# Kernel tuning notes

Hardware: AMD Instinct MI355X
Metric: run time of the kernel (lower is better)

Reference implementation:

```python
import jax, jax.numpy as jnp
import numpy as np

N, E, F, H, L, G = 100000, 1600000, 128, 128, 8, 256
EPS = 1e-5


def setup_inputs() -> dict:
    key = jax.random.key(0)
    ks = jax.random.split(key, 12)
    s = 0.05
    return {
        "x": jax.random.normal(ks[0], (N, F), jnp.float32),
        "edge_index": jax.random.randint(ks[1], (2, E), 0, N, dtype=jnp.int32),
        "batch": jnp.sort(jax.random.randint(ks[2], (N,), 0, G, dtype=jnp.int32)),
        # input projection
        "Wp": jax.random.normal(ks[3], (F, H), jnp.float32) * s,
        "bp": jnp.zeros((H,), jnp.float32),
        # stacked residual-block params (L blocks, 2 GCNConv+BN each)
        "W1": jax.random.normal(ks[4], (L, H, H), jnp.float32) * s,
        "b1": jnp.zeros((L, H), jnp.float32),
        "g1": jnp.ones((L, H), jnp.float32),
        "be1": jnp.zeros((L, H), jnp.float32),
        "W2": jax.random.normal(ks[5], (L, H, H), jnp.float32) * s,
        "b2": jnp.zeros((L, H), jnp.float32),
        "g2": jnp.ones((L, H), jnp.float32),
        "be2": jnp.zeros((L, H), jnp.float32),
        # readout MLP: 3H -> 2H -> H -> 1
        "Wa": jax.random.normal(ks[6], (3 * H, 2 * H), jnp.float32) * s,
        "ba": jnp.zeros((2 * H,), jnp.float32),
        "Wb": jax.random.normal(ks[7], (2 * H, H), jnp.float32) * s,
        "bb": jnp.zeros((H,), jnp.float32),
        "Wc": jax.random.normal(ks[8], (H, 1), jnp.float32) * s,
        "bc": jnp.zeros((1,), jnp.float32),
    }


def _bn(h, g, b):
    # BatchNorm over the node dimension (training-style batch stats, eps=1e-5)
    mu = h.mean(0)
    var = h.var(0)
    return (h - mu) * jax.lax.rsqrt(var + EPS) * g + b


def reference(x, edge_index, batch, Wp, bp, W1, b1, g1, be1, W2, b2, g2, be2,
              Wa, ba, Wb, bb, Wc, bc):
    src, dst = edge_index[0], edge_index[1]
    # GCN symmetric norm with self-loops: deg = in-degree + 1
    deg = jnp.zeros((N,), x.dtype).at[dst].add(1.0) + 1.0
    dinv = jax.lax.rsqrt(deg)
    norm_e = (dinv[src] * dinv[dst])[:, None]   # [E,1]
    self_norm = (dinv * dinv)[:, None]          # [N,1]

    def gcn(h, W, b):
        hw = h @ W                                              # [N,H]
        agg = jnp.zeros_like(hw).at[dst].add(norm_e * hw[src])  # scatter-add over edges
        return agg + self_norm * hw + b                         # self-loop + bias

    h = x @ Wp + bp

    def step(h, p):
        w1, bb1, gg1, bbe1, w2, bb2, gg2, bbe2 = p
        o = jax.nn.relu(_bn(gcn(h, w1, bb1), gg1, bbe1))
        o = _bn(gcn(o, w2, bb2), gg2, bbe2)
        return h + o, None

    h, _ = jax.lax.scan(step, h, (W1, b1, g1, be1, W2, b2, g2, be2))

    sums = jax.ops.segment_sum(h, batch, num_segments=G)
    cnt = jax.ops.segment_sum(jnp.ones((N, 1), h.dtype), batch, num_segments=G)
    mean = sums / jnp.maximum(cnt, 1.0)
    mx = jax.ops.segment_max(h, batch, num_segments=G)
    z = jnp.concatenate([mean, mx, sums], axis=1)  # [G, 3H]

    z = jax.nn.relu(z @ Wa + ba)
    z = jax.nn.relu(z @ Wb + bb)
    return z @ Wc + bc  # [G, 1]
```

## Files before the change

kernel.cpp:

```cpp
#include <hip/hip_runtime.h>
#include <hip/hip_fp16.h>
#include <math.h>
#include <float.h>

#define HDIM 128
#define NGRAPH 256
#define EPSBN 1e-5f
#define PS_REP 32
#define SLABF (2 * PS_REP * 128)

typedef _Float16 f16x8 __attribute__((ext_vector_type(8)));
typedef _Float16 f16x4 __attribute__((ext_vector_type(4)));
typedef float f32x4 __attribute__((ext_vector_type(4)));

__device__ inline unsigned enc_f(float v) {
  unsigned u = __float_as_uint(v);
  return (u & 0x80000000u) ? ~u : (u | 0x80000000u);
}
__device__ inline float dec_f(unsigned e) {
  return __uint_as_float((e & 0x80000000u) ? (e ^ 0x80000000u) : ~e);
}

__global__ void k_deg(const int* __restrict__ dst, int* __restrict__ deg, int E) {
  int i = blockIdx.x * blockDim.x + threadIdx.x;
  if (i < E) atomicAdd(&deg[dst[i]], 1);
}

__global__ void k_dinv(const int* __restrict__ deg, float* __restrict__ dinv, int n) {
  int i = blockIdx.x * blockDim.x + threadIdx.x;
  if (i < n) dinv[i] = rsqrtf((float)deg[i] + 1.0f);
}

__global__ void k_scanA(const int* __restrict__ deg, int* __restrict__ rowstart,
                        int* __restrict__ bsum, int n) {
  __shared__ int s[256];
  int t = threadIdx.x, i = blockIdx.x * 256 + t;
  int v = (i < n) ? ((deg[i] + 7) & ~7) : 0;
  s[t] = v;
  __syncthreads();
  for (int off = 1; off < 256; off <<= 1) {
    int x = (t >= off) ? s[t - off] : 0;
    __syncthreads();
    s[t] += x;
    __syncthreads();
  }
  if (i < n) rowstart[i] = s[t] - v;
  if (t == 255) bsum[blockIdx.x] = s[255];
}

__global__ void k_scanB(int* __restrict__ bsum, int nb) {
  __shared__ int s[512];
  int t = threadIdx.x;
  int v = (t < nb) ? bsum[t] : 0;
  s[t] = v;
  __syncthreads();
  for (int off = 1; off < 512; off <<= 1) {
    int x = (t >= off) ? s[t - off] : 0;
    __syncthreads();
    s[t] += x;
    __syncthreads();
  }
  if (t < nb) bsum[t] = s[t] - v;
}

__global__ void k_scanC(int* __restrict__ rowstart, const int* __restrict__ bsum,
                        const int* __restrict__ deg, int n) {
  int i = blockIdx.x * 256 + threadIdx.x;
  if (i < n) {
    int v = rowstart[i] + bsum[blockIdx.x];
    rowstart[i] = v;
    if (i == n - 1) rowstart[n] = v + ((deg[i] + 7) & ~7);
  }
}

__global__ void k_fill(const int* __restrict__ src, const int* __restrict__ dst,
                       const float* __restrict__ dinv, const int* __restrict__ prow,
                       int* __restrict__ cursor, int2* __restrict__ csr_sw, int E) {
  int e = blockIdx.x * blockDim.x + threadIdx.x;
  if (e < E) {
    int d = dst[e], s = src[e];
    int pos = prow[d] + atomicAdd(&cursor[d], 1);
    csr_sw[pos] = make_int2(s, __float_as_int(dinv[s] * dinv[d]));
  }
}

__global__ void k_pad(const int* __restrict__ deg, const int* __restrict__ prow,
                      int2* __restrict__ csr_sw, int n) {
  int i = blockIdx.x * blockDim.x + threadIdx.x;
  if (i < n) {
    int d = deg[i], dp = (d + 7) & ~7;
    int base = prow[i];
    for (int j = d; j < dp; ++j) csr_sw[base + j] = make_int2(i, 0);
  }
}

__global__ __launch_bounds__(256) void k_wprep(const float* __restrict__ W1,
                                               const float* __restrict__ W2,
                                               const float* __restrict__ Wp,
                                               _Float16* __restrict__ wt) {
  int m = blockIdx.x;
  const float* Wsrc = (m == 16) ? Wp : (((m & 1) ? W2 : W1) + (size_t)(m >> 1) * 16384);
  _Float16* Wdst = wt + (size_t)m * 16384;
  __shared__ _Float16 lds[128 * 132];
  int t = threadIdx.x;
  const float4* W4 = (const float4*)Wsrc;
  for (int it = 0; it < 16; ++it) {
    int idx = t + it * 256;
    int k = idx >> 5, c4 = idx & 31;
    float4 v = W4[idx];
    lds[(c4 * 4 + 0) * 132 + k] = (_Float16)v.x;
    lds[(c4 * 4 + 1) * 132 + k] = (_Float16)v.y;
    lds[(c4 * 4 + 2) * 132 + k] = (_Float16)v.z;
    lds[(c4 * 4 + 3) * 132 + k] = (_Float16)v.w;
  }
  __syncthreads();
  for (int it = 0; it < 16; ++it) {
    int idx = t + it * 256;
    int col = idx >> 5, k4 = idx & 31;
    f16x4 o;
    o[0] = lds[col * 132 + k4 * 4 + 0];
    o[1] = lds[col * 132 + k4 * 4 + 1];
    o[2] = lds[col * 132 + k4 * 4 + 2];
    o[3] = lds[col * 132 + k4 * 4 + 3];
    *(f16x4*)(Wdst + col * 128 + k4 * 4) = o;
  }
}

__global__ __launch_bounds__(256) void k_gemmp(const float* __restrict__ in,
                                               const _Float16* __restrict__ wt,
                                               const float* __restrict__ bias,
                                               float* __restrict__ out, int n) {
  __shared__ _Float16 As[64 * 128];
  __shared__ _Float16 Bs[128 * 128];
  char* Ap = (char*)As;
  char* Bp = (char*)Bs;
  int tid = threadIdx.x;
  int lane = tid & 63;
  int rt = tid >> 6;
  int row0 = blockIdx.x * 64;

  for (int it = 0; it < 8; ++it) {
    int idx = tid + it * 256;
    int r = idx >> 5, c4 = idx & 31;
    int row = row0 + r;
    if (row >= n) row = n - 1;
    float4 v = *(const float4*)(in + (size_t)row * 128 + c4 * 4);
    f16x4 hv;
    hv[0] = (_Float16)v.x; hv[1] = (_Float16)v.y;
    hv[2] = (_Float16)v.z; hv[3] = (_Float16)v.w;
    *(f16x4*)(Ap + ((r * 256 + c4 * 8) ^ ((r & 7) << 4))) = hv;
  }
  for (int it = 0; it < 8; ++it) {
    int idx = tid + it * 256;
    int col = idx >> 4, k8 = idx & 15;
    f16x8 v = *(const f16x8*)(wt + col * 128 + k8 * 8);
    *(f16x8*)(Bp + ((col * 256 + k8 * 16) ^ ((col & 7) << 4))) = v;
  }
  __syncthreads();

  f32x4 acc[8];
#pragma unroll
  for (int ct = 0; ct < 8; ++ct) acc[ct] = (f32x4){0.f, 0.f, 0.f, 0.f};
  int arow = rt * 16 + (lane & 15);
  int kc = (lane >> 4) * 16;
#pragma unroll
  for (int ks = 0; ks < 4; ++ks) {
    int kb = ks * 64;
    f16x8 a = *(f16x8*)(Ap + ((arow * 256 + kb + kc) ^ ((arow & 7) << 4)));
#pragma unroll
    for (int ct = 0; ct < 8; ++ct) {
      int bcol = ct * 16 + (lane & 15);
      f16x8 b = *(f16x8*)(Bp + ((bcol * 256 + kb + kc) ^ ((bcol & 7) << 4)));
      acc[ct] = __builtin_amdgcn_mfma_f32_16x16x32_f16(a, b, acc[ct], 0, 0, 0);
    }
  }

  int orow0 = row0 + rt * 16 + (lane >> 4) * 4;
#pragma unroll
  for (int ct = 0; ct < 8; ++ct) {
    int col = ct * 16 + (lane & 15);
    float bb = bias[col];
#pragma unroll
    for (int r = 0; r < 4; ++r) {
      int row = orow0 + r;
      if (row < n) out[(size_t)row * 128 + col] = acc[ct][r] + bb;
    }
  }
}

template <int XFORM>
__global__ __launch_bounds__(256) void k_gemmh(const float* __restrict__ in,
                                               const _Float16* __restrict__ wt,
                                               const float* __restrict__ psumL,
                                               const float* __restrict__ gg,
                                               const float* __restrict__ be,
                                               float* __restrict__ hres,
                                               _Float16* __restrict__ outh, int n) {
  __shared__ _Float16 As[64 * 128];
  __shared__ _Float16 Bs[128 * 128];
  __shared__ float sc_s[128], sh_s[128];
  char* Ap = (char*)As;
  char* Bp = (char*)Bs;
  int tid = threadIdx.x;
  int lane = tid & 63;
  int rt = tid >> 6;
  int row0 = blockIdx.x * 64;

  if (XFORM) {
    if (tid < 128) {
      const float* psqL = psumL + PS_REP * 128;
      float s = 0.f, q = 0.f;
#pragma unroll 8
      for (int r = 0; r < PS_REP; ++r) {
        s += psumL[r * 128 + tid];
        q += psqL[r * 128 + tid];
      }
      float mu = s / (float)n;
      float var = q / (float)n - mu * mu;
      float rs = rsqrtf(var + EPSBN);
      float sc = gg[tid] * rs;
      sc_s[tid] = sc;
      sh_s[tid] = be[tid] - mu * sc;
    }
    __syncthreads();
  }

  for (int it = 0; it < 8; ++it) {
    int idx = tid + it * 256;
    int r = idx >> 5, c4 = idx & 31;
    int rrow = row0 + r;
    int row = (rrow >= n) ? (n - 1) : rrow;
    float4 v = *(const float4*)(in + (size_t)row * 128 + c4 * 4);
    if (XFORM == 1) {
      float4 sc = *(const float4*)(sc_s + c4 * 4);
      float4 sh = *(const float4*)(sh_s + c4 * 4);
      v.x = fmaxf(v.x * sc.x + sh.x, 0.f);
      v.y = fmaxf(v.y * sc.y + sh.y, 0.f);
      v.z = fmaxf(v.z * sc.z + sh.z, 0.f);
      v.w = fmaxf(v.w * sc.w + sh.w, 0.f);
    }
    if (XFORM == 2) {
      float4 sc = *(const float4*)(sc_s + c4 * 4);
      float4 sh = *(const float4*)(sh_s + c4 * 4);
      float4 hv = *(const float4*)(hres + (size_t)row * 128 + c4 * 4);
      v.x = v.x * sc.x + sh.x + hv.x;
      v.y = v.y * sc.y + sh.y + hv.y;
      v.z = v.z * sc.z + sh.z + hv.z;
      v.w = v.w * sc.w + sh.w + hv.w;
      if (rrow < n) *(float4*)(hres + (size_t)row * 128 + c4 * 4) = v;
    }
    f16x4 hv16;
    hv16[0] = (_Float16)v.x; hv16[1] = (_Float16)v.y;
    hv16[2] = (_Float16)v.z; hv16[3] = (_Float16)v.w;
    *(f16x4*)(Ap + ((r * 256 + c4 * 8) ^ ((r & 7) << 4))) = hv16;
  }
  for (int it = 0; it < 8; ++it) {
    int idx = tid + it * 256;
    int col = idx >> 4, k8 = idx & 15;
    f16x8 v = *(const f16x8*)(wt + col * 128 + k8 * 8);
    *(f16x8*)(Bp + ((col * 256 + k8 * 16) ^ ((col & 7) << 4))) = v;
  }
  __syncthreads();

  f32x4 acc[8];
#pragma unroll
  for (int ct = 0; ct < 8; ++ct) acc[ct] = (f32x4){0.f, 0.f, 0.f, 0.f};

  int arow = rt * 16 + (lane & 15);
  int kc = (lane >> 4) * 16;
#pragma unroll
  for (int ks = 0; ks < 4; ++ks) {
    int kb = ks * 64;
    f16x8 a = *(f16x8*)(Ap + ((arow * 256 + kb + kc) ^ ((arow & 7) << 4)));
#pragma unroll
    for (int ct = 0; ct < 8; ++ct) {
      int bcol = ct * 16 + (lane & 15);
      f16x8 b = *(f16x8*)(Bp + ((bcol * 256 + kb + kc) ^ ((bcol & 7) << 4)));
      acc[ct] = __builtin_amdgcn_mfma_f32_16x16x32_f16(a, b, acc[ct], 0, 0, 0);
    }
  }

  int orow0 = row0 + rt * 16 + (lane >> 4) * 4;
#pragma unroll
  for (int ct = 0; ct < 8; ++ct) {
    int col = ct * 16 + (lane & 15);
#pragma unroll
    for (int r = 0; r < 4; ++r) {
      int row = orow0 + r;
      if (row < n) outh[(size_t)row * 128 + col] = (_Float16)acc[ct][r];
    }
  }
}

__global__ __launch_bounds__(256) void k_agg(const _Float16* __restrict__ hw,
                                             const int* __restrict__ prow,
                                             const int4* __restrict__ csr4,
                                             const float* __restrict__ dinv,
                                             const float* __restrict__ bias,
                                             float* __restrict__ out,
                                             float* __restrict__ psumL, int n) {
  int wave = threadIdx.x >> 6;
  int lane = threadIdx.x & 63;
  int grp = lane >> 4;
  int l16 = lane & 15;
  int node = blockIdx.x * 4 + wave;
  float a[8];
#pragma unroll
  for (int j = 0; j < 8; ++j) a[j] = 0.f;

  if (node < n) {
    float b8[8];
#pragma unroll
    for (int j = 0; j < 8; ++j) b8[j] = 0.f;
    int q0 = prow[node] >> 1, q1 = prow[node + 1] >> 1;
    for (int q = q0; q < q1; q += 4) {
      int4 p0 = csr4[q], p1 = csr4[q + 1], p2 = csr4[q + 2], p3 = csr4[q + 3];
      int4 pa = (grp & 2) ? p1 : p0;
      int4 pb = (grp & 2) ? p3 : p2;
      int sa = (grp & 1) ? pa.z : pa.x;
      float wa = __int_as_float((grp & 1) ? pa.w : pa.y);
      int sb = (grp & 1) ? pb.z : pb.x;
      float wb = __int_as_float((grp & 1) ? pb.w : pb.y);
      f16x8 va = *(const f16x8*)(hw + (size_t)sa * 128 + l16 * 8);
      f16x8 vb = *(const f16x8*)(hw + (size_t)sb * 128 + l16 * 8);
#pragma unroll
      for (int j = 0; j < 8; ++j) {
        a[j] += wa * (float)va[j];
        b8[j] += wb * (float)vb[j];
      }
    }
#pragma unroll
    for (int j = 0; j < 8; ++j) a[j] += b8[j];
#pragma unroll
    for (int j = 0; j < 8; ++j) {
      a[j] += __shfl_xor(a[j], 16);
      a[j] += __shfl_xor(a[j], 32);
    }
    float dn = dinv[node];
    float sn = dn * dn;
    f16x8 v = *(const f16x8*)(hw + (size_t)node * 128 + l16 * 8);
    float4 bb0 = *(const float4*)(bias + l16 * 8);
    float4 bb1 = *(const float4*)(bias + l16 * 8 + 4);
    a[0] += sn * (float)v[0] + bb0.x;
    a[1] += sn * (float)v[1] + bb0.y;
    a[2] += sn * (float)v[2] + bb0.z;
    a[3] += sn * (float)v[3] + bb0.w;
    a[4] += sn * (float)v[4] + bb1.x;
    a[5] += sn * (float)v[5] + bb1.y;
    a[6] += sn * (float)v[6] + bb1.z;
    a[7] += sn * (float)v[7] + bb1.w;
    if (grp == 0) {
      *(float4*)(out + (size_t)node * 128 + l16 * 8) = make_float4(a[0], a[1], a[2], a[3]);
      *(float4*)(out + (size_t)node * 128 + l16 * 8 + 4) = make_float4(a[4], a[5], a[6], a[7]);
    }
  }
  __shared__ float ss[4][128];
  __shared__ float sq[4][128];
  if (grp == 0) {
    bool live = (node < n);
#pragma unroll
    for (int j = 0; j < 8; ++j) {
      float v = live ? a[j] : 0.f;
      ss[wave][l16 * 8 + j] = v;
      sq[wave][l16 * 8 + j] = v * v;
    }
  }
  __syncthreads();
  int t = threadIdx.x;
  if (t < 128) {
    float s = (ss[0][t] + ss[1][t]) + (ss[2][t] + ss[3][t]);
    float q = (sq[0][t] + sq[1][t]) + (sq[2][t] + sq[3][t]);
    int rep = blockIdx.x & (PS_REP - 1);
    atomicAdd(&psumL[rep * 128 + t], s);
    atomicAdd(&psumL[PS_REP * 128 + rep * 128 + t], q);
  }
}

#define PCHUNK 128
__global__ __launch_bounds__(128) void k_pool(const float* __restrict__ h,
                                              const float* __restrict__ t2,
                                              const float* __restrict__ psumL,
                                              const float* __restrict__ gg,
                                              const float* __restrict__ be,
                                              const int* __restrict__ batch,
                                              float* __restrict__ sums,
                                              unsigned* __restrict__ maxenc,
                                              int* __restrict__ cnt, int n) {
  int c = threadIdx.x;
  __shared__ float sc_s[128], sh_s[128];
  {
    const float* psqL = psumL + PS_REP * 128;
    float s = 0.f, q = 0.f;
#pragma unroll 8
    for (int r = 0; r < PS_REP; ++r) {
      s += psumL[r * 128 + c];
      q += psqL[r * 128 + c];
    }
    float mu = s / (float)n;
    float var = q / (float)n - mu * mu;
    float rs = rsqrtf(var + EPSBN);
    float sc = gg[c] * rs;
    sc_s[c] = sc;
    sh_s[c] = be[c] - mu * sc;
  }
  __syncthreads();
  float scc = sc_s[c], shc = sh_s[c];

  int start = blockIdx.x * PCHUNK;
  if (start >= n) return;
  int end = start + PCHUNK;
  if (end > n) end = n;
  int cur = batch[start];
  float s = 0.f, mx = -FLT_MAX;
  int runlen = 0;
  for (int i = start; i < end; ++i) {
    int b = batch[i];
    if (b != cur) {
      atomicAdd(&sums[cur * 128 + c], s);
      atomicMax(&maxenc[cur * 128 + c], enc_f(mx));
      if (c == 0) atomicAdd(&cnt[cur], runlen);
      s = 0.f; mx = -FLT_MAX; runlen = 0; cur = b;
    }
    float v = h[(size_t)i * 128 + c] + scc * t2[(size_t)i * 128 + c] + shc;
    s += v;
    mx = fmaxf(mx, v);
    runlen++;
  }
  atomicAdd(&sums[cur * 128 + c], s);
  atomicMax(&maxenc[cur * 128 + c], enc_f(mx));
  if (c == 0) atomicAdd(&cnt[cur], runlen);
}

__global__ __launch_bounds__(256) void k_readout(const float* __restrict__ sums,
                                                 const unsigned* __restrict__ maxenc,
                                                 const int* __restrict__ cnt,
                                                 const float* __restrict__ Wa,
                                                 const float* __restrict__ ba,
                                                 const float* __restrict__ Wb,
                                                 const float* __restrict__ bb,
                                                 const float* __restrict__ Wc,
                                                 const float* __restrict__ bc,
                                                 float* __restrict__ out) {
  int g = blockIdx.x;
  int t = threadIdx.x;
  __shared__ float z[384];
  __shared__ float za[256];
  __shared__ float zb[128];
  float c = (float)(cnt[g] > 1 ? cnt[g] : 1);
  if (t < 128) {
    float s = sums[g * 128 + t];
    z[t] = s / c;
    z[128 + t] = dec_f(maxenc[g * 128 + t]);
    z[256 + t] = s;
  }
  __syncthreads();
  float accA = ba[t];
  for (int k = 0; k < 384; k++) accA += z[k] * Wa[k * 256 + t];
  za[t] = fmaxf(accA, 0.f);
  __syncthreads();
  if (t < 128) {
    float accB = bb[t];
    for (int k = 0; k < 256; k++) accB += za[k] * Wb[k * 128 + t];
    zb[t] = fmaxf(accB, 0.f);
  }
  __syncthreads();
  if (t < 64) {
    float p = zb[t] * Wc[t] + zb[t + 64] * Wc[t + 64];
    for (int off = 32; off > 0; off >>= 1) p += __shfl_down(p, off);
    if (t == 0) out[g] = p + bc[0];
  }
}

extern "C" void kernel_launch(void* const* d_in, const int* in_sizes, int n_in,
                              void* d_out, int out_size, void* d_ws, size_t ws_size,
                              hipStream_t stream) {
  const float* x   = (const float*)d_in[0];
  const int* edge  = (const int*)d_in[1];
  const int* batch = (const int*)d_in[2];
  const float* Wp  = (const float*)d_in[3];
  const float* bp  = (const float*)d_in[4];
  const float* W1  = (const float*)d_in[5];
  const float* b1  = (const float*)d_in[6];
  const float* g1  = (const float*)d_in[7];
  const float* be1 = (const float*)d_in[8];
  const float* W2  = (const float*)d_in[9];
  const float* b2  = (const float*)d_in[10];
  const float* g2  = (const float*)d_in[11];
  const float* be2 = (const float*)d_in[12];
  const float* Wa  = (const float*)d_in[13];
  const float* ba  = (const float*)d_in[14];
  const float* Wb  = (const float*)d_in[15];
  const float* bbp = (const float*)d_in[16];
  const float* Wc  = (const float*)d_in[17];
  const float* bc  = (const float*)d_in[18];
  float* out = (float*)d_out;

  const int N = in_sizes[0] / 128;
  const int E = in_sizes[1] / 2;
  const int* esrc = edge;
  const int* edst = edge + E;

  char* p = (char*)d_ws;
  auto carve = [&](size_t bytes) {
    char* r = p;
    p += (bytes + 255) & ~(size_t)255;
    return (void*)r;
  };
  float* h    = (float*)carve((size_t)N * 128 * 4);
  _Float16* t1h = (_Float16*)carve((size_t)N * 128 * 2);
  float* t2   = (float*)carve((size_t)N * 128 * 4);
  int2* csr_sw = (int2*)carve(((size_t)E + 8 * (size_t)N) * 8);
  int* deg     = (int*)carve((size_t)N * 4);
  float* dinv  = (float*)carve((size_t)N * 4);
  int* prow    = (int*)carve((size_t)(N + 1) * 4);
  int* cursor  = (int*)carve((size_t)N * 4);
  int* bsum    = (int*)carve(512 * 4);
  float* slab  = (float*)carve((size_t)16 * SLABF * 4);
  float* pools = (float*)carve((size_t)NGRAPH * 128 * 4);
  unsigned* poolm = (unsigned*)carve((size_t)NGRAPH * 128 * 4);
  int* poolc      = (int*)carve(NGRAPH * 4);
  _Float16* wt16  = (_Float16*)carve((size_t)17 * 128 * 128 * 2);

  const int NB = (N + 255) / 256;

  hipMemsetAsync(deg, 0, (size_t)N * 4, stream);
  hipMemsetAsync(cursor, 0, (size_t)N * 4, stream);
  hipMemsetAsync(slab, 0, (size_t)16 * SLABF * 4, stream);
  hipMemsetAsync(pools, 0, (size_t)NGRAPH * 128 * 4, stream);
  hipMemsetAsync(poolm, 0, (size_t)NGRAPH * 128 * 4, stream);
  hipMemsetAsync(poolc, 0, (size_t)NGRAPH * 4, stream);

  k_deg<<<(E + 255) / 256, 256, 0, stream>>>(edst, deg, E);
  k_dinv<<<NB, 256, 0, stream>>>(deg, dinv, N);
  k_scanA<<<NB, 256, 0, stream>>>(deg, prow, bsum, N);
  k_scanB<<<1, 512, 0, stream>>>(bsum, NB);
  k_scanC<<<NB, 256, 0, stream>>>(prow, bsum, deg, N);
  k_fill<<<(E + 255) / 256, 256, 0, stream>>>(esrc, edst, dinv, prow, cursor, csr_sw, E);
  k_pad<<<NB, 256, 0, stream>>>(deg, prow, csr_sw, N);
  k_wprep<<<17, 256, 0, stream>>>(W1, W2, Wp, wt16);

  const int GB = (N + 63) / 64;
  const int AB = (N + 3) / 4;
  const int PB = (N + PCHUNK - 1) / PCHUNK;

  k_gemmp<<<GB, 256, 0, stream>>>(x, wt16 + (size_t)16 * 16384, bp, h, N);
  k_gemmh<0><<<GB, 256, 0, stream>>>(h, wt16, nullptr, nullptr, nullptr, nullptr, t1h, N);

  for (int l = 0; l < 8; l++) {
    const _Float16* w2t = wt16 + (size_t)(l * 2 + 1) * 16384;
    float* slab1 = slab + (size_t)(2 * l) * SLABF;
    float* slab2 = slab + (size_t)(2 * l + 1) * SLABF;
    k_agg<<<AB, 256, 0, stream>>>(t1h, prow, (const int4*)csr_sw, dinv, b1 + l * 128, t2, slab1, N);
    k_gemmh<1><<<GB, 256, 0, stream>>>(t2, w2t, slab1, g1 + l * 128, be1 + l * 128, nullptr, t1h, N);
    k_agg<<<AB, 256, 0, stream>>>(t1h, prow, (const int4*)csr_sw, dinv, b2 + l * 128, t2, slab2, N);
    if (l < 7) {
      const _Float16* w1n = wt16 + (size_t)((l + 1) * 2) * 16384;
      k_gemmh<2><<<GB, 256, 0, stream>>>(t2, w1n, slab2, g2 + l * 128, be2 + l * 128, h, t1h, N);
    }
  }

  k_pool<<<PB, 128, 0, stream>>>(h, t2, slab + (size_t)15 * SLABF, g2 + 7 * 128, be2 + 7 * 128,
                                 batch, pools, poolm, poolc, N);
  k_readout<<<NGRAPH, 256, 0, stream>>>(pools, poolm, poolc, Wa, ba, Wb, bbp, Wc, bc, out);
}
```

Measured before the change: 1.873 ms.

## Store aggregation output in fp16, pad CSR rows to 4, pre-scale indices

```diff
diff --git a/kernel.cpp b/kernel.cpp
--- a/kernel.cpp
+++ b/kernel.cpp
@@ -35,7 +35,7 @@
                         int* __restrict__ bsum, int n) {
   __shared__ int s[256];
   int t = threadIdx.x, i = blockIdx.x * 256 + t;
-  int v = (i < n) ? ((deg[i] + 7) & ~7) : 0;
+  int v = (i < n) ? ((deg[i] + 3) & ~3) : 0;
   s[t] = v;
   __syncthreads();
   for (int off = 1; off < 256; off <<= 1) {
@@ -69,28 +69,28 @@
   if (i < n) {
     int v = rowstart[i] + bsum[blockIdx.x];
     rowstart[i] = v;
-    if (i == n - 1) rowstart[n] = v + ((deg[i] + 7) & ~7);
+    if (i == n - 1) rowstart[n] = v + ((deg[i] + 3) & ~3);
   }
 }
 
 __global__ void k_fill(const int* __restrict__ src, const int* __restrict__ dst,
                        const float* __restrict__ dinv, const int* __restrict__ prow,
-                       int* __restrict__ cursor, int2* __restrict__ csr_sw, int E) {
+                       int* __restrict__ cursor, int2* __restrict__ csr2, int E) {
   int e = blockIdx.x * blockDim.x + threadIdx.x;
   if (e < E) {
     int d = dst[e], s = src[e];
     int pos = prow[d] + atomicAdd(&cursor[d], 1);
-    csr_sw[pos] = make_int2(s, __float_as_int(dinv[s] * dinv[d]));
+    csr2[pos] = make_int2(s << 8, __float_as_int(dinv[s] * dinv[d]));
   }
 }
 
 __global__ void k_pad(const int* __restrict__ deg, const int* __restrict__ prow,
-                      int2* __restrict__ csr_sw, int n) {
+                      int2* __restrict__ csr2, int n) {
   int i = blockIdx.x * blockDim.x + threadIdx.x;
   if (i < n) {
-    int d = deg[i], dp = (d + 7) & ~7;
+    int d = deg[i], dp = (d + 3) & ~3;
     int base = prow[i];
-    for (int j = d; j < dp; ++j) csr_sw[base + j] = make_int2(i, 0);
+    for (int j = d; j < dp; ++j) csr2[base + j] = make_int2(i << 8, 0);
   }
 }
 
@@ -189,7 +189,7 @@
 }
 
 template <int XFORM>
-__global__ __launch_bounds__(256) void k_gemmh(const float* __restrict__ in,
+__global__ __launch_bounds__(256) void k_gemmh(const void* __restrict__ inp,
                                                const _Float16* __restrict__ wt,
                                                const float* __restrict__ psumL,
                                                const float* __restrict__ gg,
@@ -225,34 +225,57 @@
     __syncthreads();
   }
 
-  for (int it = 0; it < 8; ++it) {
-    int idx = tid + it * 256;
-    int r = idx >> 5, c4 = idx & 31;
-    int rrow = row0 + r;
-    int row = (rrow >= n) ? (n - 1) : rrow;
-    float4 v = *(const float4*)(in + (size_t)row * 128 + c4 * 4);
-    if (XFORM == 1) {
-      float4 sc = *(const float4*)(sc_s + c4 * 4);
-      float4 sh = *(const float4*)(sh_s + c4 * 4);
-      v.x = fmaxf(v.x * sc.x + sh.x, 0.f);
-      v.y = fmaxf(v.y * sc.y + sh.y, 0.f);
-      v.z = fmaxf(v.z * sc.z + sh.z, 0.f);
-      v.w = fmaxf(v.w * sc.w + sh.w, 0.f);
-    }
-    if (XFORM == 2) {
-      float4 sc = *(const float4*)(sc_s + c4 * 4);
-      float4 sh = *(const float4*)(sh_s + c4 * 4);
-      float4 hv = *(const float4*)(hres + (size_t)row * 128 + c4 * 4);
-      v.x = v.x * sc.x + sh.x + hv.x;
-      v.y = v.y * sc.y + sh.y + hv.y;
-      v.z = v.z * sc.z + sh.z + hv.z;
-      v.w = v.w * sc.w + sh.w + hv.w;
-      if (rrow < n) *(float4*)(hres + (size_t)row * 128 + c4 * 4) = v;
-    }
-    f16x4 hv16;
-    hv16[0] = (_Float16)v.x; hv16[1] = (_Float16)v.y;
-    hv16[2] = (_Float16)v.z; hv16[3] = (_Float16)v.w;
-    *(f16x4*)(Ap + ((r * 256 + c4 * 8) ^ ((r & 7) << 4))) = hv16;
+  if (XFORM == 0) {
+    const float* in = (const float*)inp;
+    for (int it = 0; it < 8; ++it) {
+      int idx = tid + it * 256;
+      int r = idx >> 5, c4 = idx & 31;
+      int row = row0 + r;
+      if (row >= n) row = n - 1;
+      float4 v = *(const float4*)(in + (size_t)row * 128 + c4 * 4);
+      f16x4 hv16;
+      hv16[0] = (_Float16)v.x; hv16[1] = (_Float16)v.y;
+      hv16[2] = (_Float16)v.z; hv16[3] = (_Float16)v.w;
+      *(f16x4*)(Ap + ((r * 256 + c4 * 8) ^ ((r & 7) << 4))) = hv16;
+    }
+  } else {
+    const _Float16* in = (const _Float16*)inp;
+    for (int it = 0; it < 4; ++it) {
+      int idx = tid + it * 256;
+      int r = idx >> 4, c8 = idx & 15;
+      int rrow = row0 + r;
+      int row = (rrow >= n) ? (n - 1) : rrow;
+      f16x8 tv = *(const f16x8*)(in + (size_t)row * 128 + c8 * 8);
+      float4 s0 = *(const float4*)(sc_s + c8 * 8);
+      float4 s1 = *(const float4*)(sc_s + c8 * 8 + 4);
+      float4 h0 = *(const float4*)(sh_s + c8 * 8);
+      float4 h1 = *(const float4*)(sh_s + c8 * 8 + 4);
+      float v[8];
+#pragma unroll
+      for (int j = 0; j < 8; ++j) v[j] = (float)tv[j];
+      v[0] = v[0] * s0.x + h0.x; v[1] = v[1] * s0.y + h0.y;
+      v[2] = v[2] * s0.z + h0.z; v[3] = v[3] * s0.w + h0.w;
+      v[4] = v[4] * s1.x + h1.x; v[5] = v[5] * s1.y + h1.y;
+      v[6] = v[6] * s1.z + h1.z; v[7] = v[7] * s1.w + h1.w;
+      if (XFORM == 1) {
+#pragma unroll
+        for (int j = 0; j < 8; ++j) v[j] = fmaxf(v[j], 0.f);
+      }
+      if (XFORM == 2) {
+        float4 hv0 = *(const float4*)(hres + (size_t)row * 128 + c8 * 8);
+        float4 hv1 = *(const float4*)(hres + (size_t)row * 128 + c8 * 8 + 4);
+        v[0] += hv0.x; v[1] += hv0.y; v[2] += hv0.z; v[3] += hv0.w;
+        v[4] += hv1.x; v[5] += hv1.y; v[6] += hv1.z; v[7] += hv1.w;
+        if (rrow < n) {
+          *(float4*)(hres + (size_t)row * 128 + c8 * 8) = make_float4(v[0], v[1], v[2], v[3]);
+          *(float4*)(hres + (size_t)row * 128 + c8 * 8 + 4) = make_float4(v[4], v[5], v[6], v[7]);
+        }
+      }
+      f16x8 o;
+#pragma unroll
+      for (int j = 0; j < 8; ++j) o[j] = (_Float16)v[j];
+      *(f16x8*)(Ap + ((r * 256 + c8 * 16) ^ ((r & 7) << 4))) = o;
+    }
   }
   for (int it = 0; it < 8; ++it) {
     int idx = tid + it * 256;
@@ -294,10 +317,10 @@
 
 __global__ __launch_bounds__(256) void k_agg(const _Float16* __restrict__ hw,
                                              const int* __restrict__ prow,
-                                             const int4* __restrict__ csr4,
+                                             const int2* __restrict__ csr2,
                                              const float* __restrict__ dinv,
                                              const float* __restrict__ bias,
-                                             float* __restrict__ out,
+                                             _Float16* __restrict__ out,
                                              float* __restrict__ psumL, int n) {
   int wave = threadIdx.x >> 6;
   int lane = threadIdx.x & 63;
@@ -309,28 +332,15 @@
   for (int j = 0; j < 8; ++j) a[j] = 0.f;
 
   if (node < n) {
-    float b8[8];
-#pragma unroll
-    for (int j = 0; j < 8; ++j) b8[j] = 0.f;
-    int q0 = prow[node] >> 1, q1 = prow[node + 1] >> 1;
-    for (int q = q0; q < q1; q += 4) {
-      int4 p0 = csr4[q], p1 = csr4[q + 1], p2 = csr4[q + 2], p3 = csr4[q + 3];
-      int4 pa = (grp & 2) ? p1 : p0;
-      int4 pb = (grp & 2) ? p3 : p2;
-      int sa = (grp & 1) ? pa.z : pa.x;
-      float wa = __int_as_float((grp & 1) ? pa.w : pa.y);
-      int sb = (grp & 1) ? pb.z : pb.x;
-      float wb = __int_as_float((grp & 1) ? pb.w : pb.y);
-      f16x8 va = *(const f16x8*)(hw + (size_t)sa * 128 + l16 * 8);
-      f16x8 vb = *(const f16x8*)(hw + (size_t)sb * 128 + l16 * 8);
-#pragma unroll
-      for (int j = 0; j < 8; ++j) {
-        a[j] += wa * (float)va[j];
-        b8[j] += wb * (float)vb[j];
-      }
-    }
-#pragma unroll
-    for (int j = 0; j < 8; ++j) a[j] += b8[j];
+    int e0 = prow[node], e1 = prow[node + 1];
+    const char* base = (const char*)hw + l16 * 16;
+    for (int e = e0; e < e1; e += 4) {
+      int2 p = csr2[e + grp];
+      float w = __int_as_float(p.y);
+      f16x8 v = *(const f16x8*)(base + (unsigned)p.x);
+#pragma unroll
+      for (int j = 0; j < 8; ++j) a[j] += w * (float)v[j];
+    }
 #pragma unroll
     for (int j = 0; j < 8; ++j) {
       a[j] += __shfl_xor(a[j], 16);
@@ -350,20 +360,24 @@
     a[6] += sn * (float)v[6] + bb1.z;
     a[7] += sn * (float)v[7] + bb1.w;
     if (grp == 0) {
-      *(float4*)(out + (size_t)node * 128 + l16 * 8) = make_float4(a[0], a[1], a[2], a[3]);
-      *(float4*)(out + (size_t)node * 128 + l16 * 8 + 4) = make_float4(a[4], a[5], a[6], a[7]);
+      f16x8 ov;
+#pragma unroll
+      for (int j = 0; j < 8; ++j) ov[j] = (_Float16)a[j];
+      *(f16x8*)(out + (size_t)node * 128 + l16 * 8) = ov;
     }
   }
   __shared__ float ss[4][128];
   __shared__ float sq[4][128];
   if (grp == 0) {
     bool live = (node < n);
-#pragma unroll
-    for (int j = 0; j < 8; ++j) {
-      float v = live ? a[j] : 0.f;
-      ss[wave][l16 * 8 + j] = v;
-      sq[wave][l16 * 8 + j] = v * v;
-    }
+    float v0 = live ? a[0] : 0.f, v1 = live ? a[1] : 0.f;
+    float v2 = live ? a[2] : 0.f, v3 = live ? a[3] : 0.f;
+    float v4 = live ? a[4] : 0.f, v5 = live ? a[5] : 0.f;
+    float v6 = live ? a[6] : 0.f, v7 = live ? a[7] : 0.f;
+    *(float4*)&ss[wave][l16 * 8] = make_float4(v0, v1, v2, v3);
+    *(float4*)&ss[wave][l16 * 8 + 4] = make_float4(v4, v5, v6, v7);
+    *(float4*)&sq[wave][l16 * 8] = make_float4(v0 * v0, v1 * v1, v2 * v2, v3 * v3);
+    *(float4*)&sq[wave][l16 * 8 + 4] = make_float4(v4 * v4, v5 * v5, v6 * v6, v7 * v7);
   }
   __syncthreads();
   int t = threadIdx.x;
@@ -378,7 +392,7 @@
 
 #define PCHUNK 128
 __global__ __launch_bounds__(128) void k_pool(const float* __restrict__ h,
-                                              const float* __restrict__ t2,
+                                              const _Float16* __restrict__ t2h,
                                               const float* __restrict__ psumL,
                                               const float* __restrict__ gg,
                                               const float* __restrict__ be,
@@ -421,7 +435,7 @@
       if (c == 0) atomicAdd(&cnt[cur], runlen);
       s = 0.f; mx = -FLT_MAX; runlen = 0; cur = b;
     }
-    float v = h[(size_t)i * 128 + c] + scc * t2[(size_t)i * 128 + c] + shc;
+    float v = h[(size_t)i * 128 + c] + scc * (float)t2h[(size_t)i * 128 + c] + shc;
     s += v;
     mx = fmaxf(mx, v);
     runlen++;
@@ -508,8 +522,8 @@
   };
   float* h    = (float*)carve((size_t)N * 128 * 4);
   _Float16* t1h = (_Float16*)carve((size_t)N * 128 * 2);
-  float* t2   = (float*)carve((size_t)N * 128 * 4);
-  int2* csr_sw = (int2*)carve(((size_t)E + 8 * (size_t)N) * 8);
+  _Float16* t2h = (_Float16*)carve((size_t)N * 128 * 2);
+  int2* csr2  = (int2*)carve(((size_t)E + 4 * (size_t)N) * 8);
   int* deg     = (int*)carve((size_t)N * 4);
   float* dinv  = (float*)carve((size_t)N * 4);
   int* prow    = (int*)carve((size_t)(N + 1) * 4);
@@ -535,8 +549,8 @@
   k_scanA<<<NB, 256, 0, stream>>>(deg, prow, bsum, N);
   k_scanB<<<1, 512, 0, stream>>>(bsum, NB);
   k_scanC<<<NB, 256, 0, stream>>>(prow, bsum, deg, N);
-  k_fill<<<(E + 255) / 256, 256, 0, stream>>>(esrc, edst, dinv, prow, cursor, csr_sw, E);
-  k_pad<<<NB, 256, 0, stream>>>(deg, prow, csr_sw, N);
+  k_fill<<<(E + 255) / 256, 256, 0, stream>>>(esrc, edst, dinv, prow, cursor, csr2, E);
+  k_pad<<<NB, 256, 0, stream>>>(deg, prow, csr2, N);
   k_wprep<<<17, 256, 0, stream>>>(W1, W2, Wp, wt16);
 
   const int GB = (N + 63) / 64;
@@ -550,16 +564,16 @@
     const _Float16* w2t = wt16 + (size_t)(l * 2 + 1) * 16384;
     float* slab1 = slab + (size_t)(2 * l) * SLABF;
     float* slab2 = slab + (size_t)(2 * l + 1) * SLABF;
-    k_agg<<<AB, 256, 0, stream>>>(t1h, prow, (const int4*)csr_sw, dinv, b1 + l * 128, t2, slab1, N);
-    k_gemmh<1><<<GB, 256, 0, stream>>>(t2, w2t, slab1, g1 + l * 128, be1 + l * 128, nullptr, t1h, N);
-    k_agg<<<AB, 256, 0, stream>>>(t1h, prow, (const int4*)csr_sw, dinv, b2 + l * 128, t2, slab2, N);
+    k_agg<<<AB, 256, 0, stream>>>(t1h, prow, csr2, dinv, b1 + l * 128, t2h, slab1, N);
+    k_gemmh<1><<<GB, 256, 0, stream>>>(t2h, w2t, slab1, g1 + l * 128, be1 + l * 128, nullptr, t1h, N);
+    k_agg<<<AB, 256, 0, stream>>>(t1h, prow, csr2, dinv, b2 + l * 128, t2h, slab2, N);
     if (l < 7) {
       const _Float16* w1n = wt16 + (size_t)((l + 1) * 2) * 16384;
-      k_gemmh<2><<<GB, 256, 0, stream>>>(t2, w1n, slab2, g2 + l * 128, be2 + l * 128, h, t1h, N);
-    }
-  }
-
-  k_pool<<<PB, 128, 0, stream>>>(h, t2, slab + (size_t)15 * SLABF, g2 + 7 * 128, be2 + 7 * 128,
+      k_gemmh<2><<<GB, 256, 0, stream>>>(t2h, w1n, slab2, g2 + l * 128, be2 + l * 128, h, t1h, N);
+    }
+  }
+
+  k_pool<<<PB, 128, 0, stream>>>(h, t2h, slab + (size_t)15 * SLABF, g2 + 7 * 128, be2 + 7 * 128,
                                  batch, pools, poolm, poolc, N);
   k_readout<<<NGRAPH, 256, 0, stream>>>(pools, poolm, poolc, Wa, ba, Wb, bbp, Wc, bc, out);
 }
```

Result: no change. 1.910 ms (+2.0%).
